# Kernel optimization log

Measured on AMD Instinct MI355X. Metric: run time of the kernel, lower is better.

Reference implementation:

```python
import jax, jax.numpy as jnp
import numpy as np

N_QUBITS = 10
DIM = 2 ** N_QUBITS
W_MUL = (2 ** 0.5) * 5 ** (-0.5)  # he_std * lrmul with gain=sqrt(2), use_wscale=True, lrmul=1
C64 = jnp.complex64


def _rx(t):
    c = jnp.cos(t / 2).astype(C64)
    s = (-1j * jnp.sin(t / 2)).astype(C64)
    return jnp.stack([jnp.stack([c, s]), jnp.stack([s, c])])


def _ry(t):
    c = jnp.cos(t / 2).astype(C64)
    s = jnp.sin(t / 2).astype(C64)
    return jnp.stack([jnp.stack([c, -s]), jnp.stack([s, c])])


def _rz(t):
    e0 = jnp.exp(-1j * t.astype(C64) / 2)
    e1 = jnp.exp(1j * t.astype(C64) / 2)
    z = jnp.zeros((), C64)
    return jnp.stack([jnp.stack([e0, z]), jnp.stack([z, e1])])


def _apply_1q(U, g, q, n):
    # left-multiply full gate (I x g x I) @ U without materializing the kron
    U = U.reshape(2 ** q, 2, -1)  # (pre, qubit, rest*cols)
    U = jnp.einsum('ab,xby->xay', g, U)
    return U.reshape(2 ** n, 2 ** n)


def _apply_cnot(U, c, t, n):
    # left-multiply CNOT(control=c, target=t) @ U; qubit 0 is most significant
    dim = 2 ** n
    T = U.reshape((2,) * n + (-1,))
    flipped = jnp.flip(T, axis=t)  # X on target
    res = jnp.stack([jnp.take(T, 0, axis=c), jnp.take(flipped, 1, axis=c)], axis=c)
    return res.reshape(dim, dim)


def _circuit_unitary(w, n):
    U = jnp.eye(2 ** n, dtype=C64)
    for q in range(n):
        U = _apply_1q(U, _rx(w[6 * q + 0]), q, n)
        U = _apply_1q(U, _ry(w[6 * q + 1]), q, n)
        U = _apply_1q(U, _rz(w[6 * q + 2]), q, n)
    for q in range(n - 1):
        U = _apply_cnot(U, q, q + 1, n)
    U = _apply_cnot(U, n - 1, 0, n)
    for q in range(n):
        U = _apply_1q(U, _rx(w[6 * q + 3]), q, n)
        U = _apply_1q(U, _ry(w[6 * q + 4]), q, n)
        U = _apply_1q(U, _rz(w[6 * q + 5]), q, n)
    return U


def _ptrace(rho, dA, dB):
    # trace out the second subsystem: (dA,dB,dA,dB) -> (dA,dA)
    return jnp.einsum('ibjb->ij', rho.reshape(dA, dB, dA, dB))


def setup_inputs() -> dict:
    key = jax.random.key(0)
    k1, k2, k3 = jax.random.split(key, 3)
    inputA = jax.random.normal(k1, (32, 32), dtype=jnp.float32)
    inputB = jax.random.normal(k2, (32, 32), dtype=jnp.float32)
    weight = jax.random.uniform(k3, (6 * N_QUBITS,), minval=0.0,
                                maxval=2 * np.pi, dtype=jnp.float32)
    return {"inputA": inputA, "inputB": inputB, "weight": weight,
            "dimA": 32, "dimB": 32}


def reference(inputA, inputB, weight, dimA, dimB):
    w = weight * W_MUL
    U = _circuit_unitary(w, N_QUBITS)
    Ud = U.conj().T
    A = inputA.astype(C64)
    B = inputB.astype(C64)
    rhoAB = jnp.kron(A, B)
    U_AB = U @ rhoAB @ Ud
    rhoBA = jnp.kron(B, A)
    U_BA = U @ rhoBA @ Ud
    mutualBatA = _ptrace(U_AB, dimA, dimB)
    mutualAatB = _ptrace(U_BA, dimB, dimA)
    return (mutualBatA, mutualAatB)
```

## Files before the change

kernel.cpp:

```cpp
#include <hip/hip_runtime.h>

#define WMUL 0.63245553203367586640f

struct cplx { float re, im; };

__device__ __forceinline__ cplx cmul(cplx a, cplx b) {
    return { a.re*b.re - a.im*b.im, a.re*b.im + a.im*b.re };
}
__device__ __forceinline__ cplx cmacc(cplx acc, cplx a, cplx b) {
    acc.re += a.re*b.re - a.im*b.im;
    acc.im += a.re*b.im + a.im*b.re;
    return acc;
}

__global__ __launch_bounds__(1024)
void qmutual_kernel(const float* __restrict__ A, const float* __restrict__ B,
                    const float* __restrict__ weight, float* __restrict__ out,
                    int out_size)
{
    __shared__ cplx arena[7744];
    cplx* CLA   = arena;
    cplx* CLB   = arena + 1024;
    cplx* CL2A  = arena + 2048;
    cplx* TA    = arena + 3072;
    cplx* TB    = arena + 4096;
    cplx* A1p   = arena + 5120;
    cplx* B1p   = arena + 6176;
    int*  invpT = (int*)(arena + 7232);
    cplx* gates = A1p;

    const int tid = threadIdx.x;
    const int i = tid >> 5, j = tid & 31;
    const int blk = blockIdx.x;
    const float* MA = blk ? B : A;
    const float* MB = blk ? A : B;

    if (tid < 20) {
        const int layer = tid / 10;
        const int q     = tid % 10;
        const float w0 = weight[6*q + 3*layer + 0] * WMUL;
        const float w1 = weight[6*q + 3*layer + 1] * WMUL;
        const float w2 = weight[6*q + 3*layer + 2] * WMUL;
        const float cx = cosf(0.5f*w0), sx = sinf(0.5f*w0);
        const float cy = cosf(0.5f*w1), sy = sinf(0.5f*w1);
        const float cz = cosf(0.5f*w2), sz = sinf(0.5f*w2);
        cplx rx[2][2] = { { {cx,0.f}, {0.f,-sx} }, { {0.f,-sx}, {cx,0.f} } };
        cplx ry[2][2] = { { {cy,0.f}, {-sy,0.f} }, { {sy,0.f}, {cy,0.f} } };
        const cplx rz0 = {cz, -sz}, rz1 = {cz, sz};
        cplx m[2][2];
        #pragma unroll
        for (int r = 0; r < 2; ++r)
            #pragma unroll
            for (int c = 0; c < 2; ++c)
                m[r][c] = cmacc(cmul(ry[r][0], rx[0][c]), ry[r][1], rx[1][c]);
        cplx* g = gates + (layer*10 + q)*4;
        g[0] = cmul(rz0, m[0][0]); g[1] = cmul(rz0, m[0][1]);
        g[2] = cmul(rz1, m[1][0]); g[3] = cmul(rz1, m[1][1]);
    }
    __syncthreads();

    {
        cplx la = {1.f,0.f}, lb = {1.f,0.f}, l2a = {1.f,0.f};
        #pragma unroll
        for (int qq = 0; qq < 5; ++qq) {
            const int rb = (j >> (4 - qq)) & 1;
            const int cb = (i >> (4 - qq)) & 1;
            la   = cmul(la,   gates[(qq     )*4 + rb*2 + cb]);
            lb   = cmul(lb,   gates[(5 + qq )*4 + rb*2 + cb]);
            l2a  = cmul(l2a,  gates[(10 + qq)*4 + rb*2 + cb]);
        }
        CLA[tid]  = { la.re,  -la.im  };
        CLB[tid]  = { lb.re,  -lb.im  };
        CL2A[tid] = { l2a.re, -l2a.im };

        const int k  = tid & 31;
        const int kb = tid >> 5;
        int x = (k << 5) | kb;
        if (x & 1) x ^= (1 << 9);
        #pragma unroll
        for (int q = 8; q >= 0; --q)
            if ((x >> (9 - q)) & 1) x ^= (1 << (8 - q));
        invpT[tid] = x;
    }
    __syncthreads();

    {
        cplx ta = {0.f,0.f}, tb = {0.f,0.f};
        #pragma unroll
        for (int k = 0; k < 32; ++k) {
            const float a_ = MA[k*32 + j];
            const float b_ = MB[k*32 + j];
            const cplx xa = CLA[k*32 + i];
            const cplx xb = CLB[k*32 + i];
            ta.re += xa.re * a_;  ta.im -= xa.im * a_;
            tb.re += xb.re * b_;  tb.im -= xb.im * b_;
        }
        TA[tid] = ta; TB[tid] = tb;
    }
    __syncthreads();

    {
        cplx a1 = {0.f,0.f}, b1 = {0.f,0.f};
        #pragma unroll
        for (int k = 0; k < 32; ++k) {
            a1 = cmacc(a1, TA[i*32 + k], CLA[k*32 + j]);
            b1 = cmacc(b1, TB[i*32 + k], CLB[k*32 + j]);
        }
        A1p[i*33 + j] = a1;
        B1p[i*33 + j] = b1;
    }
    __syncthreads();

    {
        cplx n = {0.f,0.f};
        #pragma unroll
        for (int kb = 0; kb < 32; ++kb) {
            const int l  = invpT[kb*32 + i];
            const int l2 = invpT[kb*32 + j];
            n = cmacc(n, A1p[(l >> 5)*33 + (l2 >> 5)],
                         B1p[(l & 31)*33 + (l2 & 31)]);
        }
        TA[tid] = n;
    }
    __syncthreads();

    cplx* N  = TA;
    cplx* TF = TB;
    {
        cplx tf = {0.f,0.f};
        #pragma unroll
        for (int k = 0; k < 32; ++k) {
            const cplx x = CL2A[k*32 + i];
            const cplx nk = N[k*32 + j];
            tf.re += x.re*nk.re + x.im*nk.im;
            tf.im += x.re*nk.im - x.im*nk.re;
        }
        TF[tid] = tf;
    }
    __syncthreads();

    {
        cplx r = {0.f,0.f};
        #pragma unroll
        for (int k = 0; k < 32; ++k)
            r = cmacc(r, TF[i*32 + k], CL2A[k*32 + j]);
        if (out_size >= 4096) {
            out[blk*2048 + 2*tid]     = r.re;
            out[blk*2048 + 2*tid + 1] = r.im;
        } else {
            out[blk*1024 + tid] = r.re;
        }
    }
}

extern "C" void kernel_launch(void* const* d_in, const int* in_sizes, int n_in,
                              void* d_out, int out_size, void* d_ws, size_t ws_size,
                              hipStream_t stream) {
    const float* A = (const float*)d_in[0];
    const float* B = (const float*)d_in[1];
    const float* w = (const float*)d_in[2];
    float* out = (float*)d_out;
    qmutual_kernel<<<2, 1024, 0, stream>>>(A, B, w, out, out_size);
}
```

Baseline: 74.88 us.

## Register-tile 2x2 outputs per thread with 256 threads and closed-form permutation

Each thread now computes a 2x2 output tile in every stage, and the block shrinks from 1024 to 256 threads. Shared-memory reads and writes use 16-byte vector types, and intermediates are stored transposed with padded strides. The invpT permutation table is replaced by a closed-form Gray-code index computation. The aim is more register reuse and fewer shared-memory accesses for a tiny, latency-bound two-block kernel. The cost is less parallelism and more per-thread serial work, plus extra syncs where buffers are aliased.

```diff
diff --git a/kernel.cpp b/kernel.cpp
--- a/kernel.cpp
+++ b/kernel.cpp
@@ -3,6 +3,7 @@
 #define WMUL 0.63245553203367586640f
 
 struct cplx { float re, im; };
+struct __align__(16) cplx2 { cplx a, b; };
 
 __device__ __forceinline__ cplx cmul(cplx a, cplx b) {
     return { a.re*b.re - a.im*b.im, a.re*b.im + a.im*b.re };
@@ -13,31 +14,32 @@
     return acc;
 }
 
-__global__ __launch_bounds__(1024)
+__global__ __launch_bounds__(256)
 void qmutual_kernel(const float* __restrict__ A, const float* __restrict__ B,
                     const float* __restrict__ weight, float* __restrict__ out,
                     int out_size)
 {
-    __shared__ cplx arena[7744];
+    __shared__ __align__(16) cplx arena[7360];
     cplx* CLA   = arena;
     cplx* CLB   = arena + 1024;
     cplx* CL2A  = arena + 2048;
-    cplx* TA    = arena + 3072;
-    cplx* TB    = arena + 4096;
-    cplx* A1p   = arena + 5120;
-    cplx* B1p   = arena + 6176;
-    int*  invpT = (int*)(arena + 7232);
-    cplx* gates = A1p;
+    cplx* TAT   = arena + 3072;
+    cplx* TBT   = arena + 4160;
+    cplx* A1p   = arena + 5248;
+    cplx* B1p   = arena + 6304;
+    cplx* Np    = arena;
+    cplx* TFT   = arena + 3072;
+    cplx* gates = arena + 5248;
 
     const int tid = threadIdx.x;
-    const int i = tid >> 5, j = tid & 31;
+    const int i0 = tid >> 4, j0 = tid & 15;
+    const int r0 = 2*i0, c0 = 2*j0;
     const int blk = blockIdx.x;
     const float* MA = blk ? B : A;
     const float* MB = blk ? A : B;
 
     if (tid < 20) {
-        const int layer = tid / 10;
-        const int q     = tid % 10;
+        const int layer = tid / 10, q = tid % 10;
         const float w0 = weight[6*q + 3*layer + 0] * WMUL;
         const float w1 = weight[6*q + 3*layer + 1] * WMUL;
         const float w2 = weight[6*q + 3*layer + 2] * WMUL;
@@ -53,102 +55,156 @@
             #pragma unroll
             for (int c = 0; c < 2; ++c)
                 m[r][c] = cmacc(cmul(ry[r][0], rx[0][c]), ry[r][1], rx[1][c]);
-        cplx* g = gates + (layer*10 + q)*4;
+        cplx* g = gates + tid*4;
         g[0] = cmul(rz0, m[0][0]); g[1] = cmul(rz0, m[0][1]);
         g[2] = cmul(rz1, m[1][0]); g[3] = cmul(rz1, m[1][1]);
     }
     __syncthreads();
 
     {
-        cplx la = {1.f,0.f}, lb = {1.f,0.f}, l2a = {1.f,0.f};
-        #pragma unroll
-        for (int qq = 0; qq < 5; ++qq) {
-            const int rb = (j >> (4 - qq)) & 1;
-            const int cb = (i >> (4 - qq)) & 1;
-            la   = cmul(la,   gates[(qq     )*4 + rb*2 + cb]);
-            lb   = cmul(lb,   gates[(5 + qq )*4 + rb*2 + cb]);
-            l2a  = cmul(l2a,  gates[(10 + qq)*4 + rb*2 + cb]);
-        }
-        CLA[tid]  = { la.re,  -la.im  };
-        CLB[tid]  = { lb.re,  -lb.im  };
-        CL2A[tid] = { l2a.re, -l2a.im };
-
-        const int k  = tid & 31;
-        const int kb = tid >> 5;
-        int x = (k << 5) | kb;
-        if (x & 1) x ^= (1 << 9);
-        #pragma unroll
-        for (int q = 8; q >= 0; --q)
-            if ((x >> (9 - q)) & 1) x ^= (1 << (8 - q));
-        invpT[tid] = x;
-    }
-    __syncthreads();
-
-    {
-        cplx ta = {0.f,0.f}, tb = {0.f,0.f};
-        #pragma unroll
-        for (int k = 0; k < 32; ++k) {
-            const float a_ = MA[k*32 + j];
-            const float b_ = MB[k*32 + j];
-            const cplx xa = CLA[k*32 + i];
-            const cplx xb = CLB[k*32 + i];
-            ta.re += xa.re * a_;  ta.im -= xa.im * a_;
-            tb.re += xb.re * b_;  tb.im -= xb.im * b_;
-        }
-        TA[tid] = ta; TB[tid] = tb;
-    }
-    __syncthreads();
-
-    {
-        cplx a1 = {0.f,0.f}, b1 = {0.f,0.f};
-        #pragma unroll
-        for (int k = 0; k < 32; ++k) {
-            a1 = cmacc(a1, TA[i*32 + k], CLA[k*32 + j]);
-            b1 = cmacc(b1, TB[i*32 + k], CLB[k*32 + j]);
-        }
-        A1p[i*33 + j] = a1;
-        B1p[i*33 + j] = b1;
-    }
-    __syncthreads();
-
-    {
-        cplx n = {0.f,0.f};
+        cplx vals[3][2][2];
+        #pragma unroll
+        for (int mat = 0; mat < 3; ++mat) {
+            const int gbase = (mat == 0) ? 0 : (mat == 1 ? 5 : 10);
+            #pragma unroll
+            for (int kk = 0; kk < 2; ++kk)
+                #pragma unroll
+                for (int jj = 0; jj < 2; ++jj) {
+                    const int k = r0 + kk, j = c0 + jj;
+                    cplx v = {1.f, 0.f};
+                    #pragma unroll
+                    for (int q = 0; q < 5; ++q) {
+                        const int rb = (j >> (4-q)) & 1;
+                        const int cb = (k >> (4-q)) & 1;
+                        v = cmul(v, gates[(gbase+q)*4 + rb*2 + cb]);
+                    }
+                    vals[mat][kk][jj] = { v.re, -v.im };
+                }
+        }
+        #pragma unroll
+        for (int kk = 0; kk < 2; ++kk) {
+            *(cplx2*)&CLA [(r0+kk)*32 + c0] = { vals[0][kk][0], vals[0][kk][1] };
+            *(cplx2*)&CLB [(r0+kk)*32 + c0] = { vals[1][kk][0], vals[1][kk][1] };
+            *(cplx2*)&CL2A[(r0+kk)*32 + c0] = { vals[2][kk][0], vals[2][kk][1] };
+        }
+    }
+    __syncthreads();
+
+    {
+        cplx ta[2][2] = {}, tb[2][2] = {};
+        #pragma unroll
+        for (int k = 0; k < 32; ++k) {
+            const cplx2 xa = *(const cplx2*)&CLA[k*32 + r0];
+            const cplx2 xb = *(const cplx2*)&CLB[k*32 + r0];
+            const float2 ma = *(const float2*)&MA[k*32 + c0];
+            const float2 mb = *(const float2*)&MB[k*32 + c0];
+            ta[0][0].re += xa.a.re*ma.x; ta[0][0].im -= xa.a.im*ma.x;
+            ta[0][1].re += xa.a.re*ma.y; ta[0][1].im -= xa.a.im*ma.y;
+            ta[1][0].re += xa.b.re*ma.x; ta[1][0].im -= xa.b.im*ma.x;
+            ta[1][1].re += xa.b.re*ma.y; ta[1][1].im -= xa.b.im*ma.y;
+            tb[0][0].re += xb.a.re*mb.x; tb[0][0].im -= xb.a.im*mb.x;
+            tb[0][1].re += xb.a.re*mb.y; tb[0][1].im -= xb.a.im*mb.y;
+            tb[1][0].re += xb.b.re*mb.x; tb[1][0].im -= xb.b.im*mb.x;
+            tb[1][1].re += xb.b.re*mb.y; tb[1][1].im -= xb.b.im*mb.y;
+        }
+        #pragma unroll
+        for (int g = 0; g < 2; ++g) {
+            *(cplx2*)&TAT[(c0+g)*34 + r0] = { ta[0][g], ta[1][g] };
+            *(cplx2*)&TBT[(c0+g)*34 + r0] = { tb[0][g], tb[1][g] };
+        }
+    }
+    __syncthreads();
+
+    {
+        cplx a1[2][2] = {}, b1[2][2] = {};
+        #pragma unroll
+        for (int k = 0; k < 32; ++k) {
+            const cplx2 t  = *(const cplx2*)&TAT[k*34 + r0];
+            const cplx2 u  = *(const cplx2*)&TBT[k*34 + r0];
+            const cplx2 ca = *(const cplx2*)&CLA[k*32 + c0];
+            const cplx2 cb = *(const cplx2*)&CLB[k*32 + c0];
+            a1[0][0] = cmacc(a1[0][0], t.a, ca.a); a1[0][1] = cmacc(a1[0][1], t.a, ca.b);
+            a1[1][0] = cmacc(a1[1][0], t.b, ca.a); a1[1][1] = cmacc(a1[1][1], t.b, ca.b);
+            b1[0][0] = cmacc(b1[0][0], u.a, cb.a); b1[0][1] = cmacc(b1[0][1], u.a, cb.b);
+            b1[1][0] = cmacc(b1[1][0], u.b, cb.a); b1[1][1] = cmacc(b1[1][1], u.b, cb.b);
+        }
+        #pragma unroll
+        for (int p = 0; p < 2; ++p)
+            #pragma unroll
+            for (int g = 0; g < 2; ++g) {
+                A1p[(r0+p)*33 + c0+g] = a1[p][g];
+                B1p[(r0+p)*33 + c0+g] = b1[p][g];
+            }
+    }
+    __syncthreads();
+
+    {
+        const int gr0 = r0 ^ (r0 >> 1), gr1 = (r0+1) ^ ((r0+1) >> 1);
+        const int gc0 = c0 ^ (c0 >> 1), gc1 = (c0+1) ^ ((c0+1) >> 1);
+        cplx n[2][2] = {};
         #pragma unroll
         for (int kb = 0; kb < 32; ++kb) {
-            const int l  = invpT[kb*32 + i];
-            const int l2 = invpT[kb*32 + j];
-            n = cmacc(n, A1p[(l >> 5)*33 + (l2 >> 5)],
-                         B1p[(l & 31)*33 + (l2 & 31)]);
-        }
-        TA[tid] = n;
-    }
-    __syncthreads();
-
-    cplx* N  = TA;
-    cplx* TF = TB;
-    {
-        cplx tf = {0.f,0.f};
-        #pragma unroll
-        for (int k = 0; k < 32; ++k) {
-            const cplx x = CL2A[k*32 + i];
-            const cplx nk = N[k*32 + j];
-            tf.re += x.re*nk.re + x.im*nk.im;
-            tf.im += x.re*nk.im - x.im*nk.re;
-        }
-        TF[tid] = tf;
-    }
-    __syncthreads();
-
-    {
-        cplx r = {0.f,0.f};
-        #pragma unroll
-        for (int k = 0; k < 32; ++k)
-            r = cmacc(r, TF[i*32 + k], CL2A[k*32 + j]);
+            const int t24 = (kb & 1) ? 24 : 0;
+            const int g   = kb ^ (kb >> 1);
+            const int ar0 = gr0 ^ t24, ar1 = gr1 ^ t24;
+            const int ac0 = gc0 ^ t24, ac1 = gc1 ^ t24;
+            const cplx A00 = A1p[ar0*33 + ac0], A01 = A1p[ar0*33 + ac1];
+            const cplx A10 = A1p[ar1*33 + ac0], A11 = A1p[ar1*33 + ac1];
+            const cplx B00 = B1p[g*33 + g],          B01 = B1p[g*33 + (16^g)];
+            const cplx B10 = B1p[(16^g)*33 + g],     B11 = B1p[(16^g)*33 + (16^g)];
+            n[0][0] = cmacc(n[0][0], A00, B00); n[0][1] = cmacc(n[0][1], A01, B01);
+            n[1][0] = cmacc(n[1][0], A10, B10); n[1][1] = cmacc(n[1][1], A11, B11);
+        }
+        __syncthreads();
+        #pragma unroll
+        for (int p = 0; p < 2; ++p)
+            *(cplx2*)&Np[(r0+p)*34 + c0] = { n[p][0], n[p][1] };
+    }
+    __syncthreads();
+
+    {
+        cplx tf[2][2] = {};
+        #pragma unroll
+        for (int k = 0; k < 32; ++k) {
+            const cplx2 x = *(const cplx2*)&CL2A[k*32 + r0];
+            const cplx2 m = *(const cplx2*)&Np[k*34 + c0];
+            tf[0][0].re += x.a.re*m.a.re + x.a.im*m.a.im;
+            tf[0][0].im += x.a.re*m.a.im - x.a.im*m.a.re;
+            tf[0][1].re += x.a.re*m.b.re + x.a.im*m.b.im;
+            tf[0][1].im += x.a.re*m.b.im - x.a.im*m.b.re;
+            tf[1][0].re += x.b.re*m.a.re + x.b.im*m.a.im;
+            tf[1][0].im += x.b.re*m.a.im - x.b.im*m.a.re;
+            tf[1][1].re += x.b.re*m.b.re + x.b.im*m.b.im;
+            tf[1][1].im += x.b.re*m.b.im - x.b.im*m.b.re;
+        }
+        __syncthreads();
+        #pragma unroll
+        for (int g = 0; g < 2; ++g)
+            *(cplx2*)&TFT[(c0+g)*34 + r0] = { tf[0][g], tf[1][g] };
+    }
+    __syncthreads();
+
+    {
+        cplx rr[2][2] = {};
+        #pragma unroll
+        for (int k = 0; k < 32; ++k) {
+            const cplx2 t  = *(const cplx2*)&TFT[k*34 + r0];
+            const cplx2 c2 = *(const cplx2*)&CL2A[k*32 + c0];
+            rr[0][0] = cmacc(rr[0][0], t.a, c2.a); rr[0][1] = cmacc(rr[0][1], t.a, c2.b);
+            rr[1][0] = cmacc(rr[1][0], t.b, c2.a); rr[1][1] = cmacc(rr[1][1], t.b, c2.b);
+        }
         if (out_size >= 4096) {
-            out[blk*2048 + 2*tid]     = r.re;
-            out[blk*2048 + 2*tid + 1] = r.im;
+            #pragma unroll
+            for (int p = 0; p < 2; ++p) {
+                float4 v = { rr[p][0].re, rr[p][0].im, rr[p][1].re, rr[p][1].im };
+                *(float4*)&out[blk*2048 + (r0+p)*64 + 4*j0] = v;
+            }
         } else {
-            out[blk*1024 + tid] = r.re;
+            #pragma unroll
+            for (int p = 0; p < 2; ++p) {
+                float2 v = { rr[p][0].re, rr[p][1].re };
+                *(float2*)&out[blk*1024 + (r0+p)*32 + c0] = v;
+            }
         }
     }
 }
@@ -160,5 +216,5 @@
     const float* B = (const float*)d_in[1];
     const float* w = (const float*)d_in[2];
     float* out = (float*)d_out;
-    qmutual_kernel<<<2, 1024, 0, stream>>>(A, B, w, out, out_size);
-}
+    qmutual_kernel<<<2, 256, 0, stream>>>(A, B, w, out, out_size);
+}
```

After: 74.86 us. About the same (-0.0%).
